# Performance work log

Hardware: AMD Instinct MI355X
Metric: run time of the kernel (lower is better)

Reference implementation:

```python
import jax, jax.numpy as jnp
import numpy as np

P_LEN, Q_LEN, BATCH, D, H = 300, 50, 32, 256, 256


def _make_params(key):
    ks = jax.random.split(key, 6)
    s = lambda k, shape, fan: jax.random.normal(k, shape, jnp.float32) * (1.0 / np.sqrt(fan))
    return dict(
        Wq=s(ks[0], (2, H, D), D), bq=jnp.zeros((2, H), jnp.float32),
        Wp=s(ks[1], (2, H, D), D), bp=jnp.zeros((2, H), jnp.float32),
        Wr=s(ks[2], (2, H, H), H), br=jnp.zeros((2, H), jnp.float32),
        Wg=s(ks[3], (2, H), H), bg=jnp.zeros((2,), jnp.float32),
        ln_g=jnp.ones((2, 2 * D), jnp.float32), ln_b=jnp.zeros((2, 2 * D), jnp.float32),
        W_ih=s(ks[4], (2, 4 * H, 2 * D), 2 * D), W_hh=s(ks[5], (2, 4 * H, H), H),
        b_ih=jnp.zeros((2, 4 * H), jnp.float32), b_hh=jnp.zeros((2, 4 * H), jnp.float32),
    )


def setup_inputs() -> dict:
    key = jax.random.key(0)
    k1, k2, k3, k4, kp = jax.random.split(key, 5)
    content_vec = jax.random.normal(k1, (P_LEN, BATCH, D), jnp.float32)
    question_vec = jax.random.normal(k2, (Q_LEN, BATCH, D), jnp.float32)
    p_len = jax.random.randint(k3, (BATCH,), P_LEN // 2, P_LEN + 1)
    q_len = jax.random.randint(k4, (BATCH,), Q_LEN // 2, Q_LEN + 1)
    content_mask = (jnp.arange(P_LEN)[None, :] < p_len[:, None]).astype(jnp.int32)
    question_mask = (jnp.arange(Q_LEN)[None, :] < q_len[:, None]).astype(jnp.int32)
    inp = dict(content_vec=content_vec, content_mask=content_mask,
               question_vec=question_vec, question_mask=question_mask)
    inp.update(_make_params(kp))
    return inp


def _masked_flip(v, mask):
    # v: (P, B, D); mask: (B, P). Reverses the valid prefix of each sequence,
    # leaving padding positions in place (standard Match-LSTM masked_flip).
    P = v.shape[0]
    lengths = mask.sum(axis=1)  # (B,)
    t = jnp.arange(P)[:, None]  # (P, 1)
    idx = jnp.where(t < lengths[None, :], lengths[None, :] - 1 - t, t)  # (P, B)
    idx = jnp.broadcast_to(idx[:, :, None], v.shape)
    return jnp.take_along_axis(v, idx, axis=0)


def _uni_match(cv, qv, qmask, Wq, bq, Wp, bp, Wr, br, Wg, bg, ln_g, ln_b, W_ih, W_hh, b_ih, b_hh):
    # cv: (P, B, D), qv: (Q, B, D), qmask: (B, Q)
    B = cv.shape[1]
    Hh = Wr.shape[0]
    wh = jnp.einsum('qbd,hd->qbh', qv, Wq) + bq      # (Q, B, H), precomputed once
    hp_all = jnp.einsum('pbd,hd->pbh', cv, Wp) + bp  # (P, B, H), precomputed
    pad = (qmask == 0)                               # (B, Q)

    def step(carry, xs):
        h, c = carry
        cv_t, hp_t = xs
        hr = h @ Wr.T + br                                    # (B, H)
        g = jnp.tanh(wh + hp_t[None] + hr[None])              # (Q, B, H)
        alpha = (jnp.einsum('qbh,h->qb', g, Wg) + bg).T       # (B, Q)
        alpha = jax.nn.softmax(jnp.where(pad, -jnp.inf, alpha), axis=1)
        h_alpha = jnp.einsum('bq,qbd->bd', alpha, qv)         # (B, D)
        z = jnp.concatenate([cv_t, h_alpha], axis=1)          # (B, 2D)
        mu = jnp.mean(z, axis=-1, keepdims=True)
        var = jnp.mean((z - mu) ** 2, axis=-1, keepdims=True)
        z = (z - mu) * jax.lax.rsqrt(var + 1e-5) * ln_g + ln_b
        gates = z @ W_ih.T + b_ih + h @ W_hh.T + b_hh         # (B, 4H)
        i_, f_, g_, o_ = jnp.split(gates, 4, axis=1)          # torch LSTMCell order i,f,g,o
        c_n = jax.nn.sigmoid(f_) * c + jax.nn.sigmoid(i_) * jnp.tanh(g_)
        h_n = jax.nn.sigmoid(o_) * jnp.tanh(c_n)
        return (h_n, c_n), h_n

    h0 = jnp.zeros((B, Hh), cv.dtype)
    _, hs = jax.lax.scan(step, (h0, h0), (cv, hp_all))
    return hs  # (P, B, H)


def reference(content_vec, content_mask, question_vec, question_mask,
              Wq, bq, Wp, bp, Wr, br, Wg, bg, ln_g, ln_b, W_ih, W_hh, b_ih, b_hh):
    # Dropout with p=0 (inference) is identity.
    args = lambda i: (Wq[i], bq[i], Wp[i], bp[i], Wr[i], br[i], Wg[i], bg[i],
                      ln_g[i], ln_b[i], W_ih[i], W_hh[i], b_ih[i], b_hh[i])
    right = _uni_match(content_vec, question_vec, question_mask, *args(0))
    cv_flip = _masked_flip(content_vec, content_mask)
    left = _uni_match(cv_flip, question_vec, question_mask, *args(1))
    left = _masked_flip(left, content_mask)
    res = jnp.concatenate([right, left], axis=2)            # (P, B, 2H)
    return content_mask.T[:, :, None].astype(res.dtype) * res
```

## Files before the change

### kernel.cpp

```cpp
#include <hip/hip_runtime.h>
#include <hip/hip_fp16.h>

typedef unsigned int u32;
typedef unsigned long long u64;
typedef _Float16 half2_t __attribute__((ext_vector_type(2)));
typedef _Float16 f16x8 __attribute__((ext_vector_type(8)));
typedef float f32x16 __attribute__((ext_vector_type(16)));

static constexpr int PL = 300;
static constexpr int QL = 50;
static constexpr int B  = 32;
static constexpr int D  = 256;
static constexpr int H  = 256;

__device__ __forceinline__ float fdot2(u32 w, u32 x, float acc) {
    return __builtin_amdgcn_fdot2(__builtin_bit_cast(half2_t, w),
                                  __builtin_bit_cast(half2_t, x), acc, false);
}
__device__ __forceinline__ u32 packh2(float a, float b) {
    half2_t h2; h2[0] = (_Float16)a; h2[1] = (_Float16)b;
    return __builtin_bit_cast(u32, h2);
}
__device__ __forceinline__ f32x16 mfma16(uint4 a, uint4 b, f32x16 c) {
    return __builtin_amdgcn_mfma_f32_32x32x16_f16(
        __builtin_bit_cast(f16x8, a), __builtin_bit_cast(f16x8, b), c, 0, 0, 0);
}
__device__ __forceinline__ u32 a_ld32(const u32* p) {
    return __hip_atomic_load(p, __ATOMIC_RELAXED, __HIP_MEMORY_SCOPE_AGENT);
}
__device__ __forceinline__ u64 a_ld64(const u64* p) {
    return __hip_atomic_load(p, __ATOMIC_RELAXED, __HIP_MEMORY_SCOPE_AGENT);
}
__device__ __forceinline__ void a_st32(u32* p, u32 v) {
    __hip_atomic_store(p, v, __ATOMIC_RELAXED, __HIP_MEMORY_SCOPE_AGENT);
}
__device__ __forceinline__ void a_st64(u64* p, u64 v) {
    __hip_atomic_store(p, v, __ATOMIC_RELAXED, __HIP_MEMORY_SCOPE_AGENT);
}

__global__ __launch_bounds__(256) void pack_wt3(const float* __restrict__ Whh,
                                                u32* __restrict__ dst) {
    int id = blockIdx.x * 256 + threadIdx.x;
    int u  = id & 127;
    int rw = (id >> 7) % 32;
    int j  = ((id >> 7) / 32) % 32;
    int dd = (id >> 7) / 1024;
    int R = (rw >> 3) * 256 + 8 * j + (rw & 7);
    float a = Whh[((size_t)dd * 1024 + R) * 256 + 2 * u];
    float c = Whh[((size_t)dd * 1024 + R) * 256 + 2 * u + 1];
    dst[id] = packh2(a, c);
}

__global__ __launch_bounds__(256) void pack_wr_rows(const float* __restrict__ W,
                                                    u32* __restrict__ dst) {
    int id = blockIdx.x * 256 + threadIdx.x;
    int g = id / 32768;
    int rem = id % 32768;
    int r = rem / 128, u = rem % 128;
    const float* s = &W[(g * 256 + r) * 256 + 2 * u];
    dst[id] = packh2(s[0], s[1]);
}

__global__ __launch_bounds__(256) void prep_proj(const float* __restrict__ X,
                                                 const float* __restrict__ W,
                                                 const float* __restrict__ Bv,
                                                 __half* __restrict__ out,
                                                 int T, int nt) {
    int id = blockIdx.x;
    int tb = id % nt; id /= nt;
    int b  = id % B;  id /= B;
    int g  = id;
    int t0 = tb * 8;
    int nr = T - t0; if (nr > 8) nr = 8;
    __shared__ __align__(16) float xs[8][256];
    int tid = threadIdx.x;
    for (int r = 0; r < nr; r++) xs[r][tid] = X[((t0 + r) * B + b) * D + tid];
    __syncthreads();
    const float4* wrow = (const float4*)&W[(g * H + tid) * D];
    float bb = Bv[g * H + tid];
    float acc[8];
#pragma unroll
    for (int r = 0; r < 8; r++) acc[r] = bb;
    for (int d4 = 0; d4 < D / 4; d4++) {
        float4 w = wrow[d4];
#pragma unroll
        for (int r = 0; r < 8; r++) {
            float4 x = *(const float4*)&xs[r][d4 * 4];
            acc[r] = fmaf(w.x, x.x, fmaf(w.y, x.y, fmaf(w.z, x.z, fmaf(w.w, x.w, acc[r]))));
        }
    }
    for (int r = 0; r < nr; r++)
        out[((g * B + b) * T + t0 + r) * H + tid] = __float2half(acc[r]);
}

__global__ __launch_bounds__(256) void p1_prep(const float* __restrict__ cv,
                                               const float* __restrict__ Wih,
                                               const float* __restrict__ lng,
                                               __half* __restrict__ P1) {
    int id = blockIdx.x;
    int tb = id % 38; id /= 38;
    int b  = id % 32; id /= 32;
    int dd = id;
    int t0 = tb * 8;
    int nr = PL - t0; if (nr > 8) nr = 8;
    __shared__ __align__(16) float xs[8][256];
    int tid = threadIdx.x;
    float g = lng[dd * 512 + tid];
    for (int r = 0; r < nr; r++)
        xs[r][tid] = cv[((size_t)(t0 + r) * B + b) * D + tid] * g;
    __syncthreads();
    for (int gc = 0; gc < 4; gc++) {
        int R = gc * 256 + tid;
        const float4* wrow = (const float4*)&Wih[((size_t)dd * 1024 + R) * 512];
        float acc[8] = {};
        for (int d4 = 0; d4 < 64; d4++) {
            float4 w = wrow[d4];
#pragma unroll
            for (int r = 0; r < 8; r++) {
                float4 x = *(const float4*)&xs[r][d4 * 4];
                acc[r] = fmaf(w.x, x.x, fmaf(w.y, x.y, fmaf(w.z, x.z, fmaf(w.w, x.w, acc[r]))));
            }
        }
        for (int r = 0; r < nr; r++)
            P1[((size_t)(dd * 32 + b) * PL + t0 + r) * 1024 + R] = __float2half(acc[r]);
    }
}

__global__ __launch_bounds__(256) void vp_prep(const float* __restrict__ qv,
                                               const float* __restrict__ Wih,
                                               const float* __restrict__ lng,
                                               __half* __restrict__ VP) {
    int blk = blockIdx.x;
    int dd = blk >> 8, b = (blk >> 3) & 31, rc = blk & 7;
    __shared__ __align__(16) u32 qg[50 * 128];
    __shared__ __align__(16) u32 wch[128 * 128];
    int tid = threadIdx.x;
    for (int v = tid; v < 6400; v += 256) {
        int q = v >> 7, i = v & 127;
        float a = qv[((size_t)q * 32 + b) * 256 + 2 * i]     * lng[dd * 512 + 256 + 2 * i];
        float c = qv[((size_t)q * 32 + b) * 256 + 2 * i + 1] * lng[dd * 512 + 256 + 2 * i + 1];
        qg[v] = packh2(a, c);
    }
    for (int v = tid; v < 16384; v += 256) {
        int rl = v >> 7, i = v & 127;
        int r = rc * 128 + rl;
        float a = Wih[((size_t)dd * 1024 + r) * 512 + 256 + 2 * i];
        float c = Wih[((size_t)dd * 1024 + r) * 512 + 256 + 2 * i + 1];
        wch[v] = packh2(a, c);
    }
    __syncthreads();
    for (int p = tid; p < 128 * 56; p += 256) {
        int rl = p / 56, q = p % 56;
        int r = rc * 128 + rl;
        float acc = 0.f;
        if (q < 50) {
            const u32* qr = qg + q * 128;
            const u32* wr = wch + rl * 128;
#pragma unroll 8
            for (int i = 0; i < 128; i++) acc = fdot2(wr[i], qr[i], acc);
        }
        VP[((size_t)(dd * 32 + b) * 1024 + r) * 56 + q] = __float2half(acc);
    }
}

__global__ __launch_bounds__(256) void gram_prep(const float* __restrict__ qv,
                                                 float* __restrict__ G,
                                                 float* __restrict__ qs) {
    int b = blockIdx.x;
    __shared__ float qvs[50 * 256];
    int tid = threadIdx.x;
    for (int v = tid; v < 12800; v += 256) {
        int q = v >> 8, k = v & 255;
        qvs[v] = qv[((size_t)q * 32 + b) * 256 + k];
    }
    __syncthreads();
    for (int p = tid; p < 2500; p += 256) {
        int q = p / 50, q2 = p % 50;
        float acc = 0.f;
        for (int k = 0; k < 256; k++) acc = fmaf(qvs[q * 256 + k], qvs[q2 * 256 + k], acc);
        G[((size_t)b * 50 + q) * 50 + q2] = acc;
    }
    if (tid < 52) {
        float s = 0.f;
        if (tid < 50) for (int k = 0; k < 256; k++) s += qvs[tid * 256 + k];
        qs[b * 52 + tid] = s;
    }
}

__global__ __launch_bounds__(256) void cvstats_prep(const float* __restrict__ cv,
                                                    float* __restrict__ st) {
    int blk = blockIdx.x;
    int t = blk >> 5, b = blk & 31;
    int tid = threadIdx.x;
    float v = cv[((size_t)t * 32 + b) * 256 + tid];
    float s = v, s2 = v * v;
#pragma unroll
    for (int m = 32; m; m >>= 1) { s += __shfl_xor(s, m, 64); s2 += __shfl_xor(s2, m, 64); }
    __shared__ float red[8];
    if ((tid & 63) == 0) { red[(tid >> 6) * 2] = s; red[(tid >> 6) * 2 + 1] = s2; }
    __syncthreads();
    if (tid == 0) {
        float S = red[0] + red[2] + red[4] + red[6];
        float S2 = red[1] + red[3] + red[5] + red[7];
        st[((size_t)b * 300 + t) * 2] = S;
        st[((size_t)b * 300 + t) * 2 + 1] = S2;
    }
}

__global__ __launch_bounds__(256) void c1c2_prep(const float* __restrict__ Wih,
                                                 const float* __restrict__ lng,
                                                 const float* __restrict__ lnb,
                                                 const float* __restrict__ bih,
                                                 const float* __restrict__ bhh,
                                                 float* __restrict__ C12) {
    int id = blockIdx.x * 256 + threadIdx.x;
    int dd = id >> 10, R = id & 1023;
    float s1 = 0.f, s2 = 0.f;
    const float* wr = &Wih[((size_t)dd * 1024 + R) * 512];
    for (int k = 0; k < 512; k++) {
        float w = wr[k];
        s1 = fmaf(w, lng[dd * 512 + k], s1);
        s2 = fmaf(w, lnb[dd * 512 + k], s2);
    }
    C12[(size_t)id * 2] = s1;
    C12[(size_t)id * 2 + 1] = s2 + bih[dd * 1024 + R] + bhh[dd * 1024 + R];
}

__global__ __launch_bounds__(256, 1) void scan11(
    const int*   __restrict__ cmask,
    const int*   __restrict__ qmask,
    const float* __restrict__ Wgv,
    const float* __restrict__ bgv,
    const float* __restrict__ brp,
    const u32*   __restrict__ Wtp,
    const u32*   __restrict__ Wrp,
    const __half* __restrict__ whp,
    const __half* __restrict__ hpp,
    const __half* __restrict__ P1,
    const __half* __restrict__ VP,
    const float* __restrict__ C12,
    const float* __restrict__ G,
    const float* __restrict__ qsr,
    const float* __restrict__ cvst,
    u64* __restrict__ HX,
    u32* __restrict__ B2X,
    float* __restrict__ out)
{
    int blk = blockIdx.x;
    int dd = blk >> 5, j = blk & 31;
    int tid = threadIdx.x;
    int lane = tid & 63, wave = tid >> 6;
    int rr = lane & 31, kh = lane >> 5, sw = rr & 7;

    __shared__ __align__(16) u32 sh_wt[32 * 128];
    __shared__ __align__(16) u32 sh_x[32 * 128];
    __shared__ __align__(16) u32 sh_wh[6400];
    __shared__ float sh_G[50 * 50];
    __shared__ float sh_red[4 * 32 * 33];
    __shared__ float sh_a[256];
    __shared__ float sh_af[64];
    __shared__ __align__(16) u32 sh_al2[28];
    __shared__ float sh_alpha[64];
    __shared__ float sh_qb[64];
    __shared__ float sh_qs[52];
    __shared__ float sh_r2[4];
    __shared__ float sh_cs[2];
    __shared__ int   sh_len[32];
    __shared__ __align__(16) u32 sh_hj[128];

    for (int v = tid; v < 32 * 128; v += 256) {
        int rl = v >> 7, u = v & 127;
        int c4 = u >> 2, w = u & 3;
        sh_wt[rl * 128 + (((c4 ^ (rl & 7)) << 2) | w)] =
            Wtp[((size_t)(dd * 32 + j) * 32 + rl) * 128 + u];
    }
    {
        const u32* whsrc = (const u32*)(whp + (size_t)(dd * 32 + j) * QL * H);
        for (int i = tid; i < 6400; i += 256) sh_wh[i] = whsrc[i];
    }
    for (int v = tid; v < 2500; v += 256) sh_G[v] = G[(size_t)j * 2500 + v];
    if (tid < 52) sh_qs[tid] = qsr[j * 52 + tid];
    if (tid < 64) sh_qb[tid] = (tid < QL) ? (qmask[j * QL + tid] ? 0.f : -1e30f) : -1e30f;
    if (tid < 128) sh_hj[tid] = 0;
    if (tid < 32) sh_len[tid] = 0;
    __syncthreads();
    {
        int b = tid & 31, part = tid >> 5;
        int t0 = part * 38, t1 = t0 + 38 > PL ? PL : t0 + 38;
        int s = 0;
        for (int tt = t0; tt < t1; tt++) s += cmask[b * PL + tt];
        atomicAdd(&sh_len[b], s);
    }
    __syncthreads();

    float wgr[4];
#pragma unroll
    for (int i = 0; i < 4; i++) wgr[i] = Wgv[dd * H + lane + 64 * i];
    float bgs = bgv[dd];
    float brv = brp[dd * H + tid];
    float C1r[4], C2r[4];
#pragma unroll
    for (int k = 0; k < 4; k++) {
        C1r[k] = C12[((size_t)dd * 1024 + k * 256 + tid) * 2];
        C2r[k] = C12[((size_t)dd * 1024 + k * 256 + tid) * 2 + 1];
    }
    int len_j = sh_len[j];
    float c_reg = 0.f;

    for (int t = len_j; t < PL; t++)
        out[((size_t)t * B + j) * 512 + dd * 256 + tid] = 0.f;

    if (tid < 128) a_st64(HX + (size_t)(dd * 32 + j) * 128 + tid, ((u64)1 << 32));

    const __half* hpb = hpp + (size_t)(dd * 32 + j) * PL * H;
    const u32* VPu = (const u32*)VP;
    const uint4* wr4 = (const uint4*)(Wrp + ((size_t)dd * 256 + tid) * 128);
    const u32* xrow = sh_x + rr * 128;
    const u32* wrow = sh_wt + rr * 128;

    for (int t = 0; t < PL; t++) {
        u32 want = (u32)(t + 1);
        u32 want9 = want & 511;
        int tsj = dd ? (t < len_j ? len_j - 1 - t : t) : t;
        __syncthreads();

        float p1v[4];
#pragma unroll
        for (int k = 0; k < 4; k++)
            p1v[k] = __half2float(P1[((size_t)(dd * 32 + j) * PL + tsj) * 1024 + k * 256 + tid]);
        float hpv = __half2float(hpb[(size_t)tsj * H + tid]);
        if (tid == 0) {
            sh_cs[0] = cvst[((size_t)j * 300 + tsj) * 2];
            sh_cs[1] = cvst[((size_t)j * 300 + tsj) * 2 + 1];
        }

        {
            float p0 = 0.f, p1 = 0.f, p2 = 0.f, p3 = 0.f;
#pragma unroll 8
            for (int kk = 0; kk < 32; kk++) {
                uint4 w = wr4[kk];
                uint4 hx = *(const uint4*)(sh_hj + kk * 4);
                p0 = fdot2(w.x, hx.x, p0); p1 = fdot2(w.y, hx.y, p1);
                p2 = fdot2(w.z, hx.z, p2); p3 = fdot2(w.w, hx.w, p3);
            }
            sh_a[tid] = (p0 + p1) + (p2 + p3) + brv + hpv;
        }

        {
            const u64* base = HX + (size_t)dd * 32 * 128;
            u64 v[16];
            for (;;) {
                bool ok = true;
#pragma unroll
                for (int m = 0; m < 16; m++) v[m] = a_ld64(base + m * 256 + tid);
#pragma unroll
                for (int m = 0; m < 16; m++) ok &= ((u32)(v[m] >> 32) == want);
                if (ok) break;
                __builtin_amdgcn_s_sleep(2);
            }
#pragma unroll
            for (int m = 0; m < 16; m++) {
                int w = m * 256 + tid;
                int b = w >> 7, c2 = w & 127;
                sh_x[b * 128 + (((c2 >> 2) ^ (b & 7)) << 2) + (c2 & 3)] = (u32)v[m];
            }
        }
        __syncthreads();

        {
            f32x16 acc1 = {};
#pragma unroll
            for (int kk = 0; kk < 4; kk++) {
                int c4 = wave * 8 + 2 * kk + kh;
                int pc4 = (c4 ^ sw) << 2;
                uint4 au = *(const uint4*)(xrow + pc4);
                uint4 b1 = *(const uint4*)(wrow + pc4);
                acc1 = mfma16(au, b1, acc1);
            }
#pragma unroll
            for (int q = 0; q < 16; q++) {
                int b = (q & 3) + 8 * (q >> 2) + 4 * kh;
                sh_red[(wave * 32 + b) * 33 + rr] = acc1[q];
            }
        }
        __syncthreads();

        {
            int bb = tid >> 3, rq = (tid & 7) * 4;
            u32* dst = B2X + (size_t)(dd * 32 + bb) * 1024 + j * 32 + rq;
#pragma unroll
            for (int i = 0; i < 4; i++) {
                float f = sh_red[(0 * 32 + bb) * 33 + rq + i] + sh_red[(1 * 32 + bb) * 33 + rq + i]
                        + sh_red[(2 * 32 + bb) * 33 + rq + i] + sh_red[(3 * 32 + bb) * 33 + rq + i];
                a_st32(dst + i, (__builtin_bit_cast(u32, f) & ~511u) | want9);
            }
        }

        uint4 vp[28];
#pragma unroll
        for (int k = 0; k < 4; k++) {
            const uint4* vr = (const uint4*)(VPu + ((size_t)(dd * 32 + j) * 1024 + k * 256 + tid) * 28);
#pragma unroll
            for (int i = 0; i < 7; i++) vp[k * 7 + i] = vr[i];
        }

        {
            float av[4];
#pragma unroll
            for (int i = 0; i < 4; i++) av[i] = sh_a[lane + 64 * i];
            const __half* wh16 = (const __half*)sh_wh;
            for (int q = wave; q < QL; q += 4) {
                float a = 0.f;
#pragma unroll
                for (int i = 0; i < 4; i++) {
                    float xx = (float)wh16[q * 256 + lane + 64 * i] + av[i];
                    float e = __expf(2.f * xx);
                    a = fmaf(wgr[i], (e - 1.f) / (e + 1.f), a);
                }
#pragma unroll
                for (int m = 32; m; m >>= 1) a += __shfl_xor(a, m, 64);
                if (lane == 0) sh_alpha[q] = a + bgs + sh_qb[q];
            }
        }
        __syncthreads();

        if (wave == 0) {
            float v = (lane < QL) ? sh_alpha[lane] : -1e30f;
            float m = v;
#pragma unroll
            for (int s = 32; s; s >>= 1) m = fmaxf(m, __shfl_xor(m, s, 64));
            float e = (lane < QL) ? __expf(v - m) : 0.f;
            float sum = e;
#pragma unroll
            for (int s = 32; s; s >>= 1) sum += __shfl_xor(sum, s, 64);
            float al = (lane < QL) ? e / sum : 0.f;
            sh_af[lane] = al;
            float alo = __shfl_xor(al, 1, 64);
            if (!(lane & 1) && lane < 56) sh_al2[lane >> 1] = packh2(al, alo);
        }
        __syncthreads();

        if (wave == 0) {
            float gd = 0.f;
            if (lane < QL) {
                const float* Grow = sh_G + lane * 50;
                float aq = sh_af[lane];
                for (int q2 = 0; q2 < QL; q2++) gd = fmaf(Grow[q2], sh_af[q2], gd);
                gd *= aq;
            }
#pragma unroll
            for (int m = 32; m; m >>= 1) gd += __shfl_xor(gd, m, 64);
            if (lane == 0) sh_r2[0] = gd;
        } else if (wave == 1) {
            float s = (lane < QL) ? sh_af[lane] * sh_qs[lane] : 0.f;
#pragma unroll
            for (int m = 32; m; m >>= 1) s += __shfl_xor(s, m, 64);
            if (lane == 0) sh_r2[1] = s;
        }
        __syncthreads();

        float aVP[4];
#pragma unroll
        for (int k = 0; k < 4; k++) {
            float acc = 0.f;
#pragma unroll
            for (int i = 0; i < 7; i++) {
                acc = fdot2(vp[k * 7 + i].x, sh_al2[i * 4 + 0], acc);
                acc = fdot2(vp[k * 7 + i].y, sh_al2[i * 4 + 1], acc);
                acc = fdot2(vp[k * 7 + i].z, sh_al2[i * 4 + 2], acc);
                acc = fdot2(vp[k * 7 + i].w, sh_al2[i * 4 + 3], acc);
            }
            aVP[k] = acc;
        }

        float bg2[4];
        {
            const u32* b2b = B2X + (size_t)(dd * 32 + j) * 1024 + (tid >> 3) * 32 + (tid & 7);
            u32 v0, v1, v2, v3;
            for (;;) {
                v0 = a_ld32(b2b);
                v1 = a_ld32(b2b + 8);
                v2 = a_ld32(b2b + 16);
                v3 = a_ld32(b2b + 24);
                bool ok = ((v0 & 511) == want9) & ((v1 & 511) == want9)
                        & ((v2 & 511) == want9) & ((v3 & 511) == want9);
                if (ok) break;
                __builtin_amdgcn_s_sleep(2);
            }
            bg2[0] = __builtin_bit_cast(float, v0 & ~511u);
            bg2[1] = __builtin_bit_cast(float, v1 & ~511u);
            bg2[2] = __builtin_bit_cast(float, v2 & ~511u);
            bg2[3] = __builtin_bit_cast(float, v3 & ~511u);
        }

        float hv;
        {
            float mu = (sh_cs[0] + sh_r2[1]) * (1.f / 512.f);
            float E2 = (sh_cs[1] + sh_r2[0]) * (1.f / 512.f);
            float rs = rsqrtf(E2 - mu * mu + 1e-5f);
            float gk[4];
#pragma unroll
            for (int k = 0; k < 4; k++)
                gk[k] = rs * (p1v[k] + aVP[k]) - rs * mu * C1r[k] + C2r[k] + bg2[k];
            float si = 1.f / (1.f + __expf(-gk[0]));
            float sf = 1.f / (1.f + __expf(-gk[1]));
            float so = 1.f / (1.f + __expf(-gk[3]));
            float eg = __expf(2.f * gk[2]); float tg = (eg - 1.f) / (eg + 1.f);
            float c = sf * c_reg + si * tg;
            float ec = __expf(2.f * c); float tc = (ec - 1.f) / (ec + 1.f);
            hv = so * tc;
            c_reg = c;
            float ho = __shfl_xor(hv, 1, 64);
            if (!(tid & 1)) {
                u32 pk = packh2(hv, ho);
                sh_hj[tid >> 1] = pk;
                a_st64(HX + (size_t)(dd * 32 + j) * 128 + (tid >> 1),
                       (((u64)(t + 2)) << 32) | (u64)pk);
            }
        }

        if (t < len_j)
            out[((size_t)tsj * B + j) * 512 + dd * 256 + tid] = hv;
    }
}

extern "C" void kernel_launch(void* const* d_in, const int* in_sizes, int n_in,
                              void* d_out, int out_size, void* d_ws, size_t ws_size,
                              hipStream_t stream) {
    const float* cv    = (const float*)d_in[0];
    const int*   cmask = (const int*)  d_in[1];
    const float* qv    = (const float*)d_in[2];
    const int*   qmask = (const int*)  d_in[3];
    const float* Wq    = (const float*)d_in[4];
    const float* bq    = (const float*)d_in[5];
    const float* Wp    = (const float*)d_in[6];
    const float* bp    = (const float*)d_in[7];
    const float* Wr    = (const float*)d_in[8];
    const float* br    = (const float*)d_in[9];
    const float* Wg    = (const float*)d_in[10];
    const float* bg    = (const float*)d_in[11];
    const float* ln_g  = (const float*)d_in[12];
    const float* ln_b  = (const float*)d_in[13];
    const float* Wih   = (const float*)d_in[14];
    const float* Whh   = (const float*)d_in[15];
    const float* b_ih  = (const float*)d_in[16];
    const float* b_hh  = (const float*)d_in[17];
    float* out = (float*)d_out;

    uint8_t* ws = (uint8_t*)d_ws;
    u32*    Wtp = (u32*)ws;      ws += (size_t)2 * 32 * 32 * 128 * 4;
    u32*    Wrp = (u32*)ws;      ws += (size_t)2 * 256 * 128 * 4;
    __half* VP  = (__half*)ws;   ws += (size_t)2 * 32 * 1024 * 56 * 2;
    __half* whp = (__half*)ws;   ws += (size_t)2 * 32 * 50 * 256 * 2;
    __half* hpp = (__half*)ws;   ws += (size_t)2 * 32 * 300 * 256 * 2;
    __half* P1  = (__half*)ws;   ws += (size_t)2 * 32 * 300 * 1024 * 2;
    float*  C12 = (float*)ws;    ws += (size_t)2 * 1024 * 2 * 4;
    float*  G   = (float*)ws;    ws += (size_t)32 * 50 * 50 * 4;
    float*  qs  = (float*)ws;    ws += (size_t)32 * 52 * 4;
    float*  cvs = (float*)ws;    ws += (size_t)32 * 300 * 2 * 4;
    u64* HX  = (u64*)ws;         ws += (size_t)2 * 32 * 128 * 8;
    u32* B2X = (u32*)ws;         ws += (size_t)2 * 32 * 1024 * 4;

    hipMemsetAsync(HX, 0, (size_t)2 * 32 * 128 * 8 + (size_t)2 * 32 * 1024 * 4, stream);
    hipLaunchKernelGGL(pack_wt3, dim3(1024), dim3(256), 0, stream, Whh, Wtp);
    hipLaunchKernelGGL(pack_wr_rows, dim3(256), dim3(256), 0, stream, Wr, Wrp);
    hipLaunchKernelGGL(prep_proj, dim3(2 * 32 * 7), dim3(256), 0, stream,
                       qv, Wq, bq, whp, QL, 7);
    hipLaunchKernelGGL(prep_proj, dim3(2 * 32 * 38), dim3(256), 0, stream,
                       cv, Wp, bp, hpp, PL, 38);
    hipLaunchKernelGGL(p1_prep, dim3(2 * 32 * 38), dim3(256), 0, stream,
                       cv, Wih, ln_g, P1);
    hipLaunchKernelGGL(vp_prep, dim3(512), dim3(256), 0, stream, qv, Wih, ln_g, VP);
    hipLaunchKernelGGL(gram_prep, dim3(32), dim3(256), 0, stream, qv, G, qs);
    hipLaunchKernelGGL(cvstats_prep, dim3(9600), dim3(256), 0, stream, cv, cvs);
    hipLaunchKernelGGL(c1c2_prep, dim3(8), dim3(256), 0, stream,
                       Wih, ln_g, ln_b, b_ih, b_hh, C12);
    hipLaunchKernelGGL(scan11, dim3(64), dim3(256), 0, stream,
                       cmask, qmask, Wg, bg, br, Wtp, Wrp, whp, hpp, P1, VP, C12, G, qs, cvs,
                       HX, B2X, out);
}
```

Before: 4.649 ms.

## Replace cross-block MFMA recurrence exchange with per-block local W_hh matvec

The old scan split the W_hh·h product across 32 blocks per direction. Each step exchanged hidden states and partial gate sums through global memory with spin-wait flags. The new kernel gives each block (direction, batch element) the full 1024x256 W_hh matvec for its own batch element, done with fdot2 on weights streamed from a repacked global layout. This removes the inter-block synchronisation and the spin loops, and the loop now stops at the sequence length instead of running all 300 steps. In exchange, each block reads about 512KB of fp16 weights per step from L2, making the recurrence bandwidth-bound per CU.

```diff
diff --git a/kernel.cpp b/kernel.cpp
--- a/kernel.cpp
+++ b/kernel.cpp
@@ -4,8 +4,6 @@
 typedef unsigned int u32;
 typedef unsigned long long u64;
 typedef _Float16 half2_t __attribute__((ext_vector_type(2)));
-typedef _Float16 f16x8 __attribute__((ext_vector_type(8)));
-typedef float f32x16 __attribute__((ext_vector_type(16)));
 
 static constexpr int PL = 300;
 static constexpr int QL = 50;
@@ -21,43 +19,30 @@
     half2_t h2; h2[0] = (_Float16)a; h2[1] = (_Float16)b;
     return __builtin_bit_cast(u32, h2);
 }
-__device__ __forceinline__ f32x16 mfma16(uint4 a, uint4 b, f32x16 c) {
-    return __builtin_amdgcn_mfma_f32_32x32x16_f16(
-        __builtin_bit_cast(f16x8, a), __builtin_bit_cast(f16x8, b), c, 0, 0, 0);
-}
-__device__ __forceinline__ u32 a_ld32(const u32* p) {
-    return __hip_atomic_load(p, __ATOMIC_RELAXED, __HIP_MEMORY_SCOPE_AGENT);
-}
-__device__ __forceinline__ u64 a_ld64(const u64* p) {
-    return __hip_atomic_load(p, __ATOMIC_RELAXED, __HIP_MEMORY_SCOPE_AGENT);
-}
-__device__ __forceinline__ void a_st32(u32* p, u32 v) {
-    __hip_atomic_store(p, v, __ATOMIC_RELAXED, __HIP_MEMORY_SCOPE_AGENT);
-}
-__device__ __forceinline__ void a_st64(u64* p, u64 v) {
-    __hip_atomic_store(p, v, __ATOMIC_RELAXED, __HIP_MEMORY_SCOPE_AGENT);
-}
-
-__global__ __launch_bounds__(256) void pack_wt3(const float* __restrict__ Whh,
+
+__global__ __launch_bounds__(256) void pack_whh(const float* __restrict__ Whh,
                                                 u32* __restrict__ dst) {
     int id = blockIdx.x * 256 + threadIdx.x;
-    int u  = id & 127;
-    int rw = (id >> 7) % 32;
-    int j  = ((id >> 7) / 32) % 32;
-    int dd = (id >> 7) / 1024;
-    int R = (rw >> 3) * 256 + 8 * j + (rw & 7);
-    float a = Whh[((size_t)dd * 1024 + R) * 256 + 2 * u];
-    float c = Whh[((size_t)dd * 1024 + R) * 256 + 2 * u + 1];
-    dst[id] = packh2(a, c);
-}
-
-__global__ __launch_bounds__(256) void pack_wr_rows(const float* __restrict__ W,
-                                                    u32* __restrict__ dst) {
+    int dd = id >> 17;
+    int r  = id & 131071;
+    int kc = r >> 12;
+    int R  = (r >> 2) & 1023;
+    int w  = r & 3;
+    int k  = kc * 8 + w * 2;
+    const float* s = &Whh[((size_t)dd * 1024 + R) * 256 + k];
+    dst[id] = packh2(s[0], s[1]);
+}
+
+__global__ __launch_bounds__(256) void pack_wr8(const float* __restrict__ W,
+                                                u32* __restrict__ dst) {
     int id = blockIdx.x * 256 + threadIdx.x;
-    int g = id / 32768;
-    int rem = id % 32768;
-    int r = rem / 128, u = rem % 128;
-    const float* s = &W[(g * 256 + r) * 256 + 2 * u];
+    int g  = id >> 15;
+    int r  = id & 32767;
+    int kc = r >> 10;
+    int c  = (r >> 2) & 255;
+    int w  = r & 3;
+    int k  = kc * 8 + w * 2;
+    const float* s = &W[(g * 256 + c) * 256 + k];
     dst[id] = packh2(s[0], s[1]);
 }
 
@@ -226,14 +211,14 @@
     C12[(size_t)id * 2 + 1] = s2 + bih[dd * 1024 + R] + bhh[dd * 1024 + R];
 }
 
-__global__ __launch_bounds__(256, 1) void scan11(
+__global__ __launch_bounds__(256, 1) void scan12(
     const int*   __restrict__ cmask,
     const int*   __restrict__ qmask,
     const float* __restrict__ Wgv,
     const float* __restrict__ bgv,
     const float* __restrict__ brp,
-    const u32*   __restrict__ Wtp,
-    const u32*   __restrict__ Wrp,
+    const u32*   __restrict__ WhhP,
+    const u32*   __restrict__ WrP,
     const __half* __restrict__ whp,
     const __half* __restrict__ hpp,
     const __half* __restrict__ P1,
@@ -242,21 +227,16 @@
     const float* __restrict__ G,
     const float* __restrict__ qsr,
     const float* __restrict__ cvst,
-    u64* __restrict__ HX,
-    u32* __restrict__ B2X,
     float* __restrict__ out)
 {
     int blk = blockIdx.x;
     int dd = blk >> 5, j = blk & 31;
     int tid = threadIdx.x;
     int lane = tid & 63, wave = tid >> 6;
-    int rr = lane & 31, kh = lane >> 5, sw = rr & 7;
-
-    __shared__ __align__(16) u32 sh_wt[32 * 128];
-    __shared__ __align__(16) u32 sh_x[32 * 128];
+
     __shared__ __align__(16) u32 sh_wh[6400];
     __shared__ float sh_G[50 * 50];
-    __shared__ float sh_red[4 * 32 * 33];
+    __shared__ __align__(16) u32 sh_h[128];
     __shared__ float sh_a[256];
     __shared__ float sh_af[64];
     __shared__ __align__(16) u32 sh_al2[28];
@@ -265,15 +245,8 @@
     __shared__ float sh_qs[52];
     __shared__ float sh_r2[4];
     __shared__ float sh_cs[2];
-    __shared__ int   sh_len[32];
-    __shared__ __align__(16) u32 sh_hj[128];
-
-    for (int v = tid; v < 32 * 128; v += 256) {
-        int rl = v >> 7, u = v & 127;
-        int c4 = u >> 2, w = u & 3;
-        sh_wt[rl * 128 + (((c4 ^ (rl & 7)) << 2) | w)] =
-            Wtp[((size_t)(dd * 32 + j) * 32 + rl) * 128 + u];
-    }
+    __shared__ int   sh_len1;
+
     {
         const u32* whsrc = (const u32*)(whp + (size_t)(dd * 32 + j) * QL * H);
         for (int i = tid; i < 6400; i += 256) sh_wh[i] = whsrc[i];
@@ -281,17 +254,18 @@
     for (int v = tid; v < 2500; v += 256) sh_G[v] = G[(size_t)j * 2500 + v];
     if (tid < 52) sh_qs[tid] = qsr[j * 52 + tid];
     if (tid < 64) sh_qb[tid] = (tid < QL) ? (qmask[j * QL + tid] ? 0.f : -1e30f) : -1e30f;
-    if (tid < 128) sh_hj[tid] = 0;
-    if (tid < 32) sh_len[tid] = 0;
+    if (tid < 128) sh_h[tid] = 0;
+    if (tid == 0) sh_len1 = 0;
     __syncthreads();
     {
-        int b = tid & 31, part = tid >> 5;
-        int t0 = part * 38, t1 = t0 + 38 > PL ? PL : t0 + 38;
         int s = 0;
-        for (int tt = t0; tt < t1; tt++) s += cmask[b * PL + tt];
-        atomicAdd(&sh_len[b], s);
-    }
-    __syncthreads();
+        for (int tt = tid; tt < PL; tt += 256) s += cmask[j * PL + tt];
+#pragma unroll
+        for (int m = 32; m; m >>= 1) s += __shfl_xor(s, m, 64);
+        if (lane == 0) atomicAdd(&sh_len1, s);
+    }
+    __syncthreads();
+    int len_j = sh_len1;
 
     float wgr[4];
 #pragma unroll
@@ -304,24 +278,18 @@
         C1r[k] = C12[((size_t)dd * 1024 + k * 256 + tid) * 2];
         C2r[k] = C12[((size_t)dd * 1024 + k * 256 + tid) * 2 + 1];
     }
-    int len_j = sh_len[j];
     float c_reg = 0.f;
 
     for (int t = len_j; t < PL; t++)
         out[((size_t)t * B + j) * 512 + dd * 256 + tid] = 0.f;
 
-    if (tid < 128) a_st64(HX + (size_t)(dd * 32 + j) * 128 + tid, ((u64)1 << 32));
-
     const __half* hpb = hpp + (size_t)(dd * 32 + j) * PL * H;
     const u32* VPu = (const u32*)VP;
-    const uint4* wr4 = (const uint4*)(Wrp + ((size_t)dd * 256 + tid) * 128);
-    const u32* xrow = sh_x + rr * 128;
-    const u32* wrow = sh_wt + rr * 128;
-
-    for (int t = 0; t < PL; t++) {
-        u32 want = (u32)(t + 1);
-        u32 want9 = want & 511;
-        int tsj = dd ? (t < len_j ? len_j - 1 - t : t) : t;
+    const uint4* whq = (const uint4*)WhhP + (size_t)dd * 32 * 1024;
+    const uint4* wrq = (const uint4*)WrP  + (size_t)dd * 32 * 256;
+
+    for (int t = 0; t < len_j; t++) {
+        int tsj = dd ? (len_j - 1 - t) : t;
         __syncthreads();
 
         float p1v[4];
@@ -334,67 +302,27 @@
             sh_cs[1] = cvst[((size_t)j * 300 + tsj) * 2 + 1];
         }
 
-        {
-            float p0 = 0.f, p1 = 0.f, p2 = 0.f, p3 = 0.f;
-#pragma unroll 8
-            for (int kk = 0; kk < 32; kk++) {
-                uint4 w = wr4[kk];
-                uint4 hx = *(const uint4*)(sh_hj + kk * 4);
-                p0 = fdot2(w.x, hx.x, p0); p1 = fdot2(w.y, hx.y, p1);
-                p2 = fdot2(w.z, hx.z, p2); p3 = fdot2(w.w, hx.w, p3);
-            }
-            sh_a[tid] = (p0 + p1) + (p2 + p3) + brv + hpv;
-        }
-
-        {
-            const u64* base = HX + (size_t)dd * 32 * 128;
-            u64 v[16];
-            for (;;) {
-                bool ok = true;
-#pragma unroll
-                for (int m = 0; m < 16; m++) v[m] = a_ld64(base + m * 256 + tid);
-#pragma unroll
-                for (int m = 0; m < 16; m++) ok &= ((u32)(v[m] >> 32) == want);
-                if (ok) break;
-                __builtin_amdgcn_s_sleep(2);
-            }
-#pragma unroll
-            for (int m = 0; m < 16; m++) {
-                int w = m * 256 + tid;
-                int b = w >> 7, c2 = w & 127;
-                sh_x[b * 128 + (((c2 >> 2) ^ (b & 7)) << 2) + (c2 & 3)] = (u32)v[m];
-            }
-        }
-        __syncthreads();
-
-        {
-            f32x16 acc1 = {};
-#pragma unroll
-            for (int kk = 0; kk < 4; kk++) {
-                int c4 = wave * 8 + 2 * kk + kh;
-                int pc4 = (c4 ^ sw) << 2;
-                uint4 au = *(const uint4*)(xrow + pc4);
-                uint4 b1 = *(const uint4*)(wrow + pc4);
-                acc1 = mfma16(au, b1, acc1);
-            }
-#pragma unroll
-            for (int q = 0; q < 16; q++) {
-                int b = (q & 3) + 8 * (q >> 2) + 4 * kh;
-                sh_red[(wave * 32 + b) * 33 + rr] = acc1[q];
-            }
-        }
-        __syncthreads();
-
-        {
-            int bb = tid >> 3, rq = (tid & 7) * 4;
-            u32* dst = B2X + (size_t)(dd * 32 + bb) * 1024 + j * 32 + rq;
-#pragma unroll
-            for (int i = 0; i < 4; i++) {
-                float f = sh_red[(0 * 32 + bb) * 33 + rq + i] + sh_red[(1 * 32 + bb) * 33 + rq + i]
-                        + sh_red[(2 * 32 + bb) * 33 + rq + i] + sh_red[(3 * 32 + bb) * 33 + rq + i];
-                a_st32(dst + i, (__builtin_bit_cast(u32, f) & ~511u) | want9);
-            }
-        }
+        float g0 = 0.f, g1 = 0.f, g2 = 0.f, g3 = 0.f, hr = 0.f;
+#pragma unroll 4
+        for (int kc = 0; kc < 32; kc++) {
+            uint4 hx = *(const uint4*)(sh_h + kc * 4);
+            uint4 wa = whq[kc * 1024 + tid];
+            uint4 wb = whq[kc * 1024 + 256 + tid];
+            uint4 wc = whq[kc * 1024 + 512 + tid];
+            uint4 wd = whq[kc * 1024 + 768 + tid];
+            uint4 wr = wrq[kc * 256 + tid];
+            g0 = fdot2(wa.x, hx.x, g0); g0 = fdot2(wa.y, hx.y, g0);
+            g0 = fdot2(wa.z, hx.z, g0); g0 = fdot2(wa.w, hx.w, g0);
+            g1 = fdot2(wb.x, hx.x, g1); g1 = fdot2(wb.y, hx.y, g1);
+            g1 = fdot2(wb.z, hx.z, g1); g1 = fdot2(wb.w, hx.w, g1);
+            g2 = fdot2(wc.x, hx.x, g2); g2 = fdot2(wc.y, hx.y, g2);
+            g2 = fdot2(wc.z, hx.z, g2); g2 = fdot2(wc.w, hx.w, g2);
+            g3 = fdot2(wd.x, hx.x, g3); g3 = fdot2(wd.y, hx.y, g3);
+            g3 = fdot2(wd.z, hx.z, g3); g3 = fdot2(wd.w, hx.w, g3);
+            hr = fdot2(wr.x, hx.x, hr); hr = fdot2(wr.y, hx.y, hr);
+            hr = fdot2(wr.z, hx.z, hr); hr = fdot2(wr.w, hx.w, hr);
+        }
+        sh_a[tid] = hr + brv + hpv;
 
         uint4 vp[28];
 #pragma unroll
@@ -403,6 +331,7 @@
 #pragma unroll
             for (int i = 0; i < 7; i++) vp[k * 7 + i] = vr[i];
         }
+        __syncthreads();
 
         {
             float av[4];
@@ -473,35 +402,15 @@
             aVP[k] = acc;
         }
 
-        float bg2[4];
-        {
-            const u32* b2b = B2X + (size_t)(dd * 32 + j) * 1024 + (tid >> 3) * 32 + (tid & 7);
-            u32 v0, v1, v2, v3;
-            for (;;) {
-                v0 = a_ld32(b2b);
-                v1 = a_ld32(b2b + 8);
-                v2 = a_ld32(b2b + 16);
-                v3 = a_ld32(b2b + 24);
-                bool ok = ((v0 & 511) == want9) & ((v1 & 511) == want9)
-                        & ((v2 & 511) == want9) & ((v3 & 511) == want9);
-                if (ok) break;
-                __builtin_amdgcn_s_sleep(2);
-            }
-            bg2[0] = __builtin_bit_cast(float, v0 & ~511u);
-            bg2[1] = __builtin_bit_cast(float, v1 & ~511u);
-            bg2[2] = __builtin_bit_cast(float, v2 & ~511u);
-            bg2[3] = __builtin_bit_cast(float, v3 & ~511u);
-        }
-
         float hv;
         {
             float mu = (sh_cs[0] + sh_r2[1]) * (1.f / 512.f);
             float E2 = (sh_cs[1] + sh_r2[0]) * (1.f / 512.f);
             float rs = rsqrtf(E2 - mu * mu + 1e-5f);
-            float gk[4];
+            float gk[4] = { g0, g1, g2, g3 };
 #pragma unroll
             for (int k = 0; k < 4; k++)
-                gk[k] = rs * (p1v[k] + aVP[k]) - rs * mu * C1r[k] + C2r[k] + bg2[k];
+                gk[k] += rs * (p1v[k] + aVP[k]) - rs * mu * C1r[k] + C2r[k];
             float si = 1.f / (1.f + __expf(-gk[0]));
             float sf = 1.f / (1.f + __expf(-gk[1]));
             float so = 1.f / (1.f + __expf(-gk[3]));
@@ -511,16 +420,10 @@
             hv = so * tc;
             c_reg = c;
             float ho = __shfl_xor(hv, 1, 64);
-            if (!(tid & 1)) {
-                u32 pk = packh2(hv, ho);
-                sh_hj[tid >> 1] = pk;
-                a_st64(HX + (size_t)(dd * 32 + j) * 128 + (tid >> 1),
-                       (((u64)(t + 2)) << 32) | (u64)pk);
-            }
-        }
-
-        if (t < len_j)
-            out[((size_t)tsj * B + j) * 512 + dd * 256 + tid] = hv;
+            if (!(tid & 1)) sh_h[tid >> 1] = packh2(hv, ho);
+        }
+
+        out[((size_t)tsj * B + j) * 512 + dd * 256 + tid] = hv;
     }
 }
 
@@ -548,8 +451,8 @@
     float* out = (float*)d_out;
 
     uint8_t* ws = (uint8_t*)d_ws;
-    u32*    Wtp = (u32*)ws;      ws += (size_t)2 * 32 * 32 * 128 * 4;
-    u32*    Wrp = (u32*)ws;      ws += (size_t)2 * 256 * 128 * 4;
+    u32*    WhhP = (u32*)ws;     ws += (size_t)2 * 32 * 1024 * 4 * 4;
+    u32*    WrP  = (u32*)ws;     ws += (size_t)2 * 32 * 256 * 4 * 4;
     __half* VP  = (__half*)ws;   ws += (size_t)2 * 32 * 1024 * 56 * 2;
     __half* whp = (__half*)ws;   ws += (size_t)2 * 32 * 50 * 256 * 2;
     __half* hpp = (__half*)ws;   ws += (size_t)2 * 32 * 300 * 256 * 2;
@@ -557,13 +460,10 @@
     float*  C12 = (float*)ws;    ws += (size_t)2 * 1024 * 2 * 4;
     float*  G   = (float*)ws;    ws += (size_t)32 * 50 * 50 * 4;
     float*  qs  = (float*)ws;    ws += (size_t)32 * 52 * 4;
-    float*  cvs = (float*)ws;    ws += (size_t)32 * 300 * 2 * 4;
-    u64* HX  = (u64*)ws;         ws += (size_t)2 * 32 * 128 * 8;
-    u32* B2X = (u32*)ws;         ws += (size_t)2 * 32 * 1024 * 4;
-
-    hipMemsetAsync(HX, 0, (size_t)2 * 32 * 128 * 8 + (size_t)2 * 32 * 1024 * 4, stream);
-    hipLaunchKernelGGL(pack_wt3, dim3(1024), dim3(256), 0, stream, Whh, Wtp);
-    hipLaunchKernelGGL(pack_wr_rows, dim3(256), dim3(256), 0, stream, Wr, Wrp);
+    float*  cvs = (float*)ws;
+
+    hipLaunchKernelGGL(pack_whh, dim3(1024), dim3(256), 0, stream, Whh, WhhP);
+    hipLaunchKernelGGL(pack_wr8, dim3(256), dim3(256), 0, stream, Wr, WrP);
     hipLaunchKernelGGL(prep_proj, dim3(2 * 32 * 7), dim3(256), 0, stream,
                        qv, Wq, bq, whp, QL, 7);
     hipLaunchKernelGGL(prep_proj, dim3(2 * 32 * 38), dim3(256), 0, stream,
@@ -575,7 +475,7 @@
     hipLaunchKernelGGL(cvstats_prep, dim3(9600), dim3(256), 0, stream, cv, cvs);
     hipLaunchKernelGGL(c1c2_prep, dim3(8), dim3(256), 0, stream,
                        Wih, ln_g, ln_b, b_ih, b_hh, C12);
-    hipLaunchKernelGGL(scan11, dim3(64), dim3(256), 0, stream,
-                       cmask, qmask, Wg, bg, br, Wtp, Wrp, whp, hpp, P1, VP, C12, G, qs, cvs,
-                       HX, B2X, out);
-}
+    hipLaunchKernelGGL(scan12, dim3(64), dim3(256), 0, stream,
+                       cmask, qmask, Wg, bg, br, WhhP, WrP, whp, hpp, P1, VP, C12, G, qs, cvs,
+                       out);
+}
```

Result: no change. 4.640 ms (-0.2%).
